# Kernel optimization log

Hardware: AMD Instinct MI355X
Metric: run time of the kernel (lower is better)

## Reference

```python
import jax, jax.numpy as jnp
import numpy as np
import math

B, N, DQ, DK, DV, H = 8, 1024, 512, 512, 512, 8


def setup_inputs() -> dict:
    key = jax.random.key(0)
    ks = jax.random.split(key, 9)
    s = 0.02
    return {
        "Q": jax.random.normal(ks[0], (B, N, DQ), jnp.float32),
        "K": jax.random.normal(ks[1], (B, N, DK), jnp.float32),
        "mask": jax.random.bernoulli(ks[2], 0.9, (B, N)).astype(jnp.float32),
        "Wq": jax.random.normal(ks[3], (DQ, DV), jnp.float32) * s,
        "bq": jnp.zeros((DV,), jnp.float32),
        "Wk": jax.random.normal(ks[4], (DK, DV), jnp.float32) * s,
        "bk": jnp.zeros((DV,), jnp.float32),
        "Wv": jax.random.normal(ks[5], (DK, DV), jnp.float32) * s,
        "bv": jnp.zeros((DV,), jnp.float32),
        "Wo": jax.random.normal(ks[6], (DV, DV), jnp.float32) * s,
        "bo": jnp.zeros((DV,), jnp.float32),
    }


def reference(Q, K, mask, Wq, bq, Wk, bk, Wv, bv, Wo, bo):
    b, n, _ = Q.shape
    dV = Wq.shape[1]
    dh = dV // H
    scale = 1.0 / math.sqrt(dV)
    m = mask[..., None]                      # [B,N,1]
    Qp = (Q @ Wq + bq) * m                   # [B,N,dV]
    Kp = (K @ Wk + bk) * m
    Vp = (K @ Wv + bv) * m
    # torch.cat(x.split(dh,2),0) == head-major stacking -> keep as [H,B,N,dh]
    q = Qp.reshape(b, n, H, dh).transpose(2, 0, 1, 3)
    k = Kp.reshape(b, n, H, dh).transpose(2, 0, 1, 3)
    v = Vp.reshape(b, n, H, dh).transpose(2, 0, 1, 3)
    S = jnp.einsum('hbnd,hbmd->hbnm', q, k) * scale   # [H,B,N,N]
    mx = jnp.max(S, axis=3, keepdims=True)            # unmasked row max (faithful)
    m1 = mask[None, :, :, None]                       # [1,B,N,1]
    m2 = mask[None, :, None, :]                       # [1,B,1,N]
    num = jnp.exp((S - mx) * m1 * m2) * m1 * m2
    A = num / (jnp.sum(num, axis=3, keepdims=True) + 1e-16)
    O = q + jnp.einsum('hbnm,hbmd->hbnd', A, v)       # residual on Q_
    O = O.transpose(1, 2, 0, 3).reshape(b, n, dV)     # un-split heads
    O = O + jax.nn.relu((O @ Wo + bo) * m)
    return O
```

## Files before the change

kernel.cpp:

```cpp
#include <hip/hip_runtime.h>

typedef short bf16x8 __attribute__((ext_vector_type(8)));
typedef float f32x4 __attribute__((ext_vector_type(4)));
typedef float f32x16 __attribute__((ext_vector_type(16)));

#define MFMA16(a, b, c) __builtin_amdgcn_mfma_f32_16x16x32_bf16((a), (b), (c), 0, 0, 0)
#define MFMA32(a, b, c) __builtin_amdgcn_mfma_f32_32x32x16_bf16((a), (b), (c), 0, 0, 0)

#define GLOAD_LDS16(g, l)                                              \
  __builtin_amdgcn_global_load_lds(                                    \
      (const __attribute__((address_space(1))) unsigned int*)(g),      \
      (__attribute__((address_space(3))) unsigned int*)(l), 16, 0, 0)

__device__ __forceinline__ unsigned short f2b(float f) {
  union { float f; unsigned int u; } x; x.f = f;
  unsigned int r = x.u + 0x7FFFu + ((x.u >> 16) & 1u);
  return (unsigned short)(r >> 16);
}
__device__ __forceinline__ float b2f(unsigned short h) {
  union { unsigned int u; float f; } x; x.u = ((unsigned int)h) << 16;
  return x.f;
}
__device__ __forceinline__ unsigned int cvtpk(float lo, float hi) {
  unsigned int r;
  asm("v_cvt_pk_bf16_f32 %0, %1, %2" : "=v"(r) : "v"(lo), "v"(hi));
  return r;
}
__device__ __forceinline__ short cvt1(float x) {
  return (short)(unsigned short)cvtpk(x, x);
}
__device__ __forceinline__ float vexp2(float x) {
  float r;
  asm("v_exp_f32 %0, %1" : "=v"(r) : "v"(x));
  return r;
}

#define SCALE2 0.06375870724f

__global__ __launch_bounds__(256) void prep_kernel(
    const float* __restrict__ Wq, const float* __restrict__ Wk,
    const float* __restrict__ Wv, const float* __restrict__ Wo,
    const float* __restrict__ Q, const float* __restrict__ K,
    const float* __restrict__ mask,
    short* __restrict__ Wt, short* __restrict__ Qb, short* __restrict__ Kb,
    short* __restrict__ mbf) {
  __shared__ float tile[64][65];
  const int bid = blockIdx.x;
  const int t = threadIdx.x;
  if (bid < 256) {
    const int z = bid >> 6;
    const int rem = bid & 63;
    const int k0 = (rem >> 3) * 64, n0 = (rem & 7) * 64;
    const float* W = (z == 0) ? Wq : (z == 1) ? Wk : (z == 2) ? Wv : Wo;
    const float ws = (z == 1) ? SCALE2 : 1.0f;
    const int r = t >> 4, cc = (t & 15) * 4;
#pragma unroll
    for (int it = 0; it < 4; ++it) {
      int row = r + it * 16;
      const float4 v = *(const float4*)(W + (k0 + row) * 512 + n0 + cc);
      tile[row][cc + 0] = v.x; tile[row][cc + 1] = v.y;
      tile[row][cc + 2] = v.z; tile[row][cc + 3] = v.w;
    }
    __syncthreads();
    short* out = Wt + z * (512 * 512);
#pragma unroll
    for (int it = 0; it < 4; ++it) {
      int nrow = r + it * 16;
      unsigned int u0 = cvtpk(tile[cc + 0][nrow] * ws, tile[cc + 1][nrow] * ws);
      unsigned int u1 = cvtpk(tile[cc + 2][nrow] * ws, tile[cc + 3][nrow] * ws);
      uint2 uv; uv.x = u0; uv.y = u1;
      *(uint2*)(out + (n0 + nrow) * 512 + k0 + cc) = uv;
    }
  } else {
    const int idx = bid - 256;
    const int ybit = idx >> 11;
    const int x = idx & 2047;
    if (ybit == 0 && x < 4) {
      int i = (x * 256 + t) * 8;
      float4 a = *(const float4*)(mask + i);
      float4 bb = *(const float4*)(mask + i + 4);
      unsigned int m0 = (a.x != 0.f) ? 0x3F80u : 0u;
      unsigned int m1 = (a.y != 0.f) ? 0x3F80u : 0u;
      unsigned int m2 = (a.z != 0.f) ? 0x3F80u : 0u;
      unsigned int m3 = (a.w != 0.f) ? 0x3F80u : 0u;
      unsigned int m4 = (bb.x != 0.f) ? 0x3F80u : 0u;
      unsigned int m5 = (bb.y != 0.f) ? 0x3F80u : 0u;
      unsigned int m6 = (bb.z != 0.f) ? 0x3F80u : 0u;
      unsigned int m7 = (bb.w != 0.f) ? 0x3F80u : 0u;
      uint4 mm;
      mm.x = m0 | (m1 << 16); mm.y = m2 | (m3 << 16);
      mm.z = m4 | (m5 << 16); mm.w = m6 | (m7 << 16);
      *(uint4*)(mbf + i) = mm;
    }
    const float* src = ybit ? K : Q;
    short* dst = ybit ? Kb : Qb;
    int i = (x * 256 + t) * 8;
    float4 v0 = *(const float4*)(src + i);
    float4 v1 = *(const float4*)(src + i + 4);
    uint2 a, b;
    a.x = cvtpk(v0.x, v0.y); a.y = cvtpk(v0.z, v0.w);
    b.x = cvtpk(v1.x, v1.y); b.y = cvtpk(v1.z, v1.w);
    *(uint2*)(dst + i) = a;
    *(uint2*)(dst + i + 4) = b;
  }
}

__device__ __forceinline__ void gemm_bf16_core(
    const short* __restrict__ A, const short* __restrict__ Wt,
    short* Lb, int m0, int t, f32x4 acc[4][4]) {
  const int lane = t & 63, w = t >> 6;
  const int c = lane & 15, g = lane >> 4;
  const int wr = w >> 1, wc = w & 1;
  const int lr = lane >> 3;
  const int sswz = ((lane & 7) ^ lr) << 3;
  const int swc = (c & 7) << 3;
  short* Al = Lb;
  short* Bl = Lb + 8192;

  for (int kt = 0; kt < 8; ++kt) {
#pragma unroll
    for (int it = 0; it < 4; ++it) {
      int row = w * 32 + it * 8;
      GLOAD_LDS16(A + (size_t)(m0 + row + lr) * 512 + kt * 64 + sswz, Al + row * 64);
      GLOAD_LDS16(Wt + (size_t)(row + lr) * 512 + kt * 64 + sswz, Bl + row * 64);
    }
    __syncthreads();
    __builtin_amdgcn_s_setprio(1);
#pragma unroll
    for (int kc = 0; kc < 2; ++kc) {
      bf16x8 af[4], bfr[4];
#pragma unroll
      for (int mi = 0; mi < 4; ++mi) {
        int r = wr * 64 + mi * 16 + c;
        af[mi] = *(const bf16x8*)(Al + r * 64 + ((kc * 32 + 8 * g) ^ swc));
      }
#pragma unroll
      for (int ni = 0; ni < 4; ++ni) {
        int r = wc * 64 + ni * 16 + c;
        bfr[ni] = *(const bf16x8*)(Bl + r * 64 + ((kc * 32 + 8 * g) ^ swc));
      }
#pragma unroll
      for (int mi = 0; mi < 4; ++mi)
#pragma unroll
        for (int ni = 0; ni < 4; ++ni)
          acc[mi][ni] = MFMA16(af[mi], bfr[ni], acc[mi][ni]);
    }
    __builtin_amdgcn_s_setprio(0);
    __syncthreads();
  }
}

__global__ __launch_bounds__(256) void proj2_kernel(
    const short* __restrict__ Qb, const short* __restrict__ Kb,
    const short* __restrict__ Wt4,
    const float* __restrict__ bq, const float* __restrict__ bk, const float* __restrict__ bv,
    const float* __restrict__ maskf,
    short* __restrict__ Qp, short* __restrict__ Kp, short* __restrict__ Vt) {
  __shared__ short Lbuf[16384];
  const int by = blockIdx.y;
  const int m0 = blockIdx.x * 128;
  const int t = threadIdx.x;
  const short* A;
  const short* Wt;
  const float* bias;
  int nbase;
  if (by < 4) { A = Qb; nbase = by * 128; Wt = Wt4 + nbase * 512; bias = bq; }
  else if (by < 8) { A = Kb; nbase = (by - 4) * 128; Wt = Wt4 + 262144 + nbase * 512; bias = bk; }
  else { A = Kb; nbase = (by - 8) * 128; Wt = Wt4 + 524288 + nbase * 512; bias = bv; }
  const float bscale = (by >= 4 && by < 8) ? SCALE2 : 1.0f;

  const f32x4 zz = {0.f, 0.f, 0.f, 0.f};
  f32x4 acc[4][4];
#pragma unroll
  for (int mi = 0; mi < 4; ++mi)
#pragma unroll
    for (int ni = 0; ni < 4; ++ni) acc[mi][ni] = zz;
  gemm_bf16_core(A, Wt, Lbuf, m0, t, acc);

  const int lane = t & 63, w = t >> 6;
  const int c = lane & 15, g = lane >> 4;
  const int wr = w >> 1, wc = w & 1;
  float mk[4][4];
#pragma unroll
  for (int mi = 0; mi < 4; ++mi) {
    int mbase = m0 + wr * 64 + mi * 16 + 4 * g;
#pragma unroll
    for (int i = 0; i < 4; ++i) mk[mi][i] = maskf[mbase + i];
  }
  float bval[4];
#pragma unroll
  for (int ni = 0; ni < 4; ++ni) bval[ni] = bias[nbase + wc * 64 + ni * 16 + c] * bscale;

  if (by < 8) {
#pragma unroll
    for (int ni = 0; ni < 4; ++ni) {
      int nloc = wc * 64 + ni * 16 + c;
#pragma unroll
      for (int mi = 0; mi < 4; ++mi) {
#pragma unroll
        for (int i = 0; i < 4; ++i) {
          int mloc = wr * 64 + mi * 16 + 4 * g + i;
          float v = (acc[mi][ni][i] + bval[ni]) * mk[mi][i];
          Lbuf[mloc * 128 + (nloc ^ ((mloc & 7) << 3))] = cvt1(v);
        }
      }
    }
    __syncthreads();
    short* outp = (by < 4) ? Qp : Kp;
    const int rrow = t >> 4, rcol = (t & 15) * 8;
#pragma unroll
    for (int p = 0; p < 8; ++p) {
      int m = p * 16 + rrow;
      bf16x8 vv = *(const bf16x8*)(Lbuf + m * 128 + (rcol ^ ((m & 7) << 3)));
      *(bf16x8*)(outp + (size_t)(m0 + m) * 512 + nbase + rcol) = vv;
    }
  } else {
#pragma unroll
    for (int ni = 0; ni < 4; ++ni) {
      int nloc = wc * 64 + ni * 16 + c;
#pragma unroll
      for (int mi = 0; mi < 4; ++mi) {
        int mloc4 = wr * 64 + mi * 16 + 4 * g;
        unsigned int lo = cvtpk((acc[mi][ni][0] + bval[ni]) * mk[mi][0],
                                (acc[mi][ni][1] + bval[ni]) * mk[mi][1]);
        unsigned int hi = cvtpk((acc[mi][ni][2] + bval[ni]) * mk[mi][2],
                                (acc[mi][ni][3] + bval[ni]) * mk[mi][3]);
        int ma = (mloc4 & 15) + (((mloc4 >> 4) ^ (nloc & 7)) << 4);
        uint2 uv; uv.x = lo; uv.y = hi;
        *(uint2*)(Lbuf + nloc * 128 + ma) = uv;
      }
    }
    __syncthreads();
    const int rrow = t >> 4, rcol = (t & 15) * 8;
#pragma unroll
    for (int p = 0; p < 8; ++p) {
      int n = p * 16 + rrow;
      int ma = (rcol & 8) + (((rcol >> 4) ^ (n & 7)) << 4);
      bf16x8 vv = *(const bf16x8*)(Lbuf + n * 128 + ma);
      int d = nbase + n;
      int hh = d >> 6, dd = d & 63;
      int mg = m0 + rcol;
      int bi = mg >> 10, seq0 = mg & 1023;
      *(bf16x8*)(Vt + ((size_t)((bi * 8 + hh) * 64 + dd)) * 1024 + seq0) = vv;
    }
  }
}

__global__ __launch_bounds__(256, 4) void attn8_kernel(
    const short* __restrict__ Qp, const short* __restrict__ Kp,
    const short* __restrict__ Vt, const float* __restrict__ mask,
    const short* __restrict__ mbf, short* __restrict__ Obb) {
  __shared__ short Kl[2][32 * 128];
  __shared__ short Vl[2][32 * 128];
  __shared__ short Ml[1024];
  const int t = threadIdx.x, lane = t & 63, w = t >> 6;
  const int q32 = lane & 31, hi = lane >> 5;
  const int hw = blockIdx.x;
  const int L = (hw & 7) * 64 + (hw >> 3);
  const int qt = L & 7, head = L >> 3;
  const int b = head & 7, h = head >> 3;
  const int n0 = qt * 128 + w * 32;

  const short* Kg = Kp + (size_t)(b * 1024) * 512 + h * 64;
  const short* Vg = Vt + (size_t)((b * 8 + h) * 64) * 1024;

  bf16x8 qf[4];
  {
    const short* qptr = Qp + ((size_t)(b * 1024 + n0 + q32) * 512 + h * 64 + 8 * hi);
#pragma unroll
    for (int kk = 0; kk < 4; ++kk) qf[kk] = *(const bf16x8*)(qptr + 16 * kk);
  }
  asm volatile("s_waitcnt vmcnt(0)" ::: "memory");
  __builtin_amdgcn_sched_barrier(0);

  auto STAGE = [&](int kvt, int buf) {
    const int kr = kvt * 64;
    short* Kd = &Kl[buf][0];
    short* Vd = &Vl[buf][0];
#pragma unroll
    for (int it = 0; it < 2; ++it) {
      int rb = it * 16 + w * 4;
      int r2 = rb + (lane >> 4);
      int sx = (lane & 15) ^ (r2 & 15);
      GLOAD_LDS16(Kg + (size_t)(kr + 2 * r2 + (sx >> 3)) * 512 + (sx & 7) * 8, Kd + rb * 128);
    }
#pragma unroll
    for (int it = 0; it < 2; ++it) {
      int rb = it * 16 + w * 4;
      int rv = rb + (lane >> 4);
      int sx = (lane & 15) ^ (rv & 15);
      GLOAD_LDS16(Vg + (size_t)(2 * rv + (sx >> 3)) * 1024 + kr + (sx & 7) * 8, Vd + rb * 128);
    }
  };

  if (w < 2) GLOAD_LDS16(mbf + b * 1024 + w * 512 + lane * 8, Ml + w * 512);
  STAGE(0, 0);
  STAGE(1, 1);

  f32x16 o0, o1, suma;
#pragma unroll
  for (int e = 0; e < 16; ++e) { o0[e] = 0.f; o1[e] = 0.f; suma[e] = 0.f; }

#pragma unroll 1
  for (int kvt = 0; kvt < 16; ++kvt) {
    const int cur = kvt & 1;
    if (kvt < 15) { asm volatile("s_waitcnt vmcnt(4)" ::: "memory"); }
    else          { asm volatile("s_waitcnt vmcnt(0)" ::: "memory"); }
    __builtin_amdgcn_sched_barrier(0);
    __builtin_amdgcn_s_barrier();
    __builtin_amdgcn_sched_barrier(0);

#pragma unroll
    for (int half = 0; half < 2; ++half) {
      bf16x8 ka[4], va[2][2], mo[2];
      {
        const int kvr = 32 * half + q32;
        const int r2 = kvr >> 1;
#pragma unroll
        for (int kk = 0; kk < 4; ++kk) {
          int sx = ((((kvr & 1) << 3) | (2 * kk + hi)) ^ (r2 & 15));
          ka[kk] = *(const bf16x8*)(&Kl[cur][0] + r2 * 128 + sx * 8);
        }
      }
#pragma unroll
      for (int ds = 0; ds < 2; ++ds) {
        const int d = 32 * ds + q32;
        const int rv = d >> 1;
#pragma unroll
        for (int ch = 0; ch < 2; ++ch) {
          int sx = ((((d & 1) << 3) | (4 * half + 2 * ch + hi)) ^ (rv & 15));
          va[ds][ch] = *(const bf16x8*)(&Vl[cur][0] + rv * 128 + sx * 8);
        }
      }
#pragma unroll
      for (int ch = 0; ch < 2; ++ch)
        mo[ch] = *(const bf16x8*)(Ml + kvt * 64 + 32 * half + 16 * ch + 8 * hi);

      __builtin_amdgcn_sched_barrier(0);
      asm volatile("s_waitcnt lgkmcnt(0)" ::: "memory");
      __builtin_amdgcn_sched_barrier(0);
      if (half == 1) {
        __builtin_amdgcn_s_barrier();
        __builtin_amdgcn_sched_barrier(0);
        if (kvt < 14) STAGE(kvt + 2, cur);
        __builtin_amdgcn_sched_barrier(0);
      }

      f32x16 s0;
#pragma unroll
      for (int e = 0; e < 16; ++e) s0[e] = 0.f;
      __builtin_amdgcn_s_setprio(1);
#pragma unroll
      for (int kk = 0; kk < 4; ++kk) s0 = MFMA32(ka[kk], qf[kk], s0);
      __builtin_amdgcn_s_setprio(0);

      f32x16 p0;
#pragma unroll
      for (int e = 0; e < 16; ++e) p0[e] = vexp2(s0[e]);

      bf16x8 pf[2];
#pragma unroll
      for (int ch = 0; ch < 2; ++ch) {
        unsigned int w01a = cvtpk(p0[8 * ch + 0], p0[8 * ch + 1]);
        unsigned int w01b = cvtpk(p0[8 * ch + 2], p0[8 * ch + 3]);
        unsigned int w23a = cvtpk(p0[8 * ch + 4], p0[8 * ch + 5]);
        unsigned int w23b = cvtpk(p0[8 * ch + 6], p0[8 * ch + 7]);
        unsigned int x0 = hi ? w01a : w23a;
        unsigned int x1 = hi ? w01b : w23b;
        unsigned int g0 = (unsigned int)__shfl_xor((int)x0, 32);
        unsigned int g1 = (unsigned int)__shfl_xor((int)x1, 32);
        union { unsigned int u[4]; bf16x8 v; } pu;
        pu.u[0] = hi ? g0 : w01a;
        pu.u[1] = hi ? g1 : w01b;
        pu.u[2] = hi ? w23a : g0;
        pu.u[3] = hi ? w23b : g1;
        pf[ch] = pu.v;
      }

      __builtin_amdgcn_s_setprio(1);
#pragma unroll
      for (int ch = 0; ch < 2; ++ch) {
        o0 = MFMA32(va[0][ch], pf[ch], o0);
        o1 = MFMA32(va[1][ch], pf[ch], o1);
        suma = MFMA32(mo[ch], pf[ch], suma);
      }
      __builtin_amdgcn_s_setprio(0);
    }
  }

  __builtin_amdgcn_s_barrier();
  __builtin_amdgcn_sched_barrier(0);
  short* Tw = (w < 2) ? (&Kl[0][0] + w * 2304) : (&Vl[0][0] + (w - 2) * 2304);
  const float inv = __builtin_amdgcn_rcpf(suma[0] + 1e-16f);
#pragma unroll
  for (int rr = 0; rr < 4; ++rr) {
    uint2 uv0, uv1;
    uv0.x = cvtpk(o0[4 * rr + 0] * inv, o0[4 * rr + 1] * inv);
    uv0.y = cvtpk(o0[4 * rr + 2] * inv, o0[4 * rr + 3] * inv);
    *(uint2*)(Tw + q32 * 68 + 8 * rr + 4 * hi) = uv0;
    uv1.x = cvtpk(o1[4 * rr + 0] * inv, o1[4 * rr + 1] * inv);
    uv1.y = cvtpk(o1[4 * rr + 2] * inv, o1[4 * rr + 3] * inv);
    *(uint2*)(Tw + q32 * 68 + 32 + 8 * rr + 4 * hi) = uv1;
  }
  asm volatile("s_waitcnt lgkmcnt(0)" ::: "memory");
  __builtin_amdgcn_sched_barrier(0);

  const int erow = lane >> 1, ecs = (lane & 1) * 8;
  const float mk1 = mask[b * 1024 + n0 + erow];
#pragma unroll
  for (int it = 0; it < 4; ++it) {
    int col = ecs + it * 16;
    bf16x8 av = *(const bf16x8*)(Tw + erow * 68 + col);
    const short* qptr = Qp + (size_t)(b * 1024 + n0 + erow) * 512 + h * 64 + col;
    bf16x8 qv = *(const bf16x8*)qptr;
    uint4 rr;
    rr.x = cvtpk(b2f((unsigned short)qv[0]) + mk1 * b2f((unsigned short)av[0]),
                 b2f((unsigned short)qv[1]) + mk1 * b2f((unsigned short)av[1]));
    rr.y = cvtpk(b2f((unsigned short)qv[2]) + mk1 * b2f((unsigned short)av[2]),
                 b2f((unsigned short)qv[3]) + mk1 * b2f((unsigned short)av[3]));
    rr.z = cvtpk(b2f((unsigned short)qv[4]) + mk1 * b2f((unsigned short)av[4]),
                 b2f((unsigned short)qv[5]) + mk1 * b2f((unsigned short)av[5]));
    rr.w = cvtpk(b2f((unsigned short)qv[6]) + mk1 * b2f((unsigned short)av[6]),
                 b2f((unsigned short)qv[7]) + mk1 * b2f((unsigned short)av[7]));
    *(uint4*)(Obb + (size_t)(b * 1024 + n0 + erow) * 512 + h * 64 + col) = rr;
  }
}

__global__ __launch_bounds__(256) void final2_kernel(
    const short* __restrict__ Obb,
    const short* __restrict__ Wto, const float* __restrict__ bo,
    const float* __restrict__ maskf, float* __restrict__ out) {
  __shared__ short Lbuf[16384];
  const int m0 = blockIdx.x * 128, n0 = blockIdx.y * 128;
  const int t = threadIdx.x;
  const f32x4 zz = {0.f, 0.f, 0.f, 0.f};
  f32x4 acc[4][4];
#pragma unroll
  for (int mi = 0; mi < 4; ++mi)
#pragma unroll
    for (int ni = 0; ni < 4; ++ni) acc[mi][ni] = zz;
  gemm_bf16_core(Obb, Wto + n0 * 512, Lbuf, m0, t, acc);

  const int lane = t & 63, w = t >> 6;
  const int c = lane & 15, g = lane >> 4;
  const int wr = w >> 1, wc = w & 1;
  float mk[4][4];
#pragma unroll
  for (int mi = 0; mi < 4; ++mi) {
    int mbase = m0 + wr * 64 + mi * 16 + 4 * g;
#pragma unroll
    for (int i = 0; i < 4; ++i) mk[mi][i] = maskf[mbase + i];
  }
#pragma unroll
  for (int ni = 0; ni < 4; ++ni) {
    int n = n0 + wc * 64 + ni * 16 + c;
    float bval = bo[n];
#pragma unroll
    for (int mi = 0; mi < 4; ++mi) {
      int mbase = m0 + wr * 64 + mi * 16 + 4 * g;
#pragma unroll
      for (int i = 0; i < 4; ++i) {
        float v = (acc[mi][ni][i] + bval) * mk[mi][i];
        v = fmaxf(v, 0.f);
        size_t off = (size_t)(mbase + i) * 512 + n;
        out[off] = b2f((unsigned short)Obb[off]) + v;
      }
    }
  }
}

extern "C" void kernel_launch(void* const* d_in, const int* in_sizes, int n_in,
                              void* d_out, int out_size, void* d_ws, size_t ws_size,
                              hipStream_t stream) {
  (void)in_sizes; (void)n_in; (void)out_size; (void)ws_size;
  const float* Q    = (const float*)d_in[0];
  const float* K    = (const float*)d_in[1];
  const float* mask = (const float*)d_in[2];
  const float* Wq   = (const float*)d_in[3];
  const float* bq   = (const float*)d_in[4];
  const float* Wk   = (const float*)d_in[5];
  const float* bk   = (const float*)d_in[6];
  const float* Wv   = (const float*)d_in[7];
  const float* bv   = (const float*)d_in[8];
  const float* Wo   = (const float*)d_in[9];
  const float* bo   = (const float*)d_in[10];

  char* ws = (char*)d_ws;
  const size_t MB = 1048576;
  short* Wt4 = (short*)ws;
  short* Qb  = (short*)(ws + 2 * MB);
  short* Kb  = (short*)(ws + 10 * MB);
  short* Qp  = (short*)(ws + 18 * MB);
  short* Kp  = (short*)(ws + 26 * MB);
  short* Vt  = (short*)(ws + 34 * MB);
  short* Obb = (short*)(ws + 42 * MB);
  short* mbf = (short*)(ws + 50 * MB);
  float* out = (float*)d_out;

  prep_kernel<<<dim3(4352), 256, 0, stream>>>(Wq, Wk, Wv, Wo, Q, K, mask, Wt4, Qb, Kb, mbf);
  proj2_kernel<<<dim3(64, 12), 256, 0, stream>>>(Qb, Kb, Wt4, bq, bk, bv, mask, Qp, Kp, Vt);
  attn8_kernel<<<dim3(512), 256, 0, stream>>>(Qp, Kp, Vt, mask, mbf, Obb);
  final2_kernel<<<dim3(64, 4), 256, 0, stream>>>(Obb, Wt4 + 3 * 262144, bo, mask, out);
}
```

Measured before the change: 90.96 us.

## Split attention KV range across two waves per 32-query block

The attention kernel now uses 128-thread blocks that each handle 32 queries, with the two waves splitting the 1024-key range in half (split-K). Each wave stages its own K/V tiles into a private LDS buffer. It prefetches only one tile ahead and needs no block barriers in the main loop. Partial O and row-sum accumulators are combined through LDS at the end. This gives 4x more blocks and removes intra-loop barriers, at the cost of re-reading Q-independent K/V per 32 queries (4x more K/V traffic), a shallower prefetch, and an extra reduction step.

```diff
diff --git a/kernel.cpp b/kernel.cpp
--- a/kernel.cpp
+++ b/kernel.cpp
@@ -246,23 +246,25 @@
   }
 }
 
-__global__ __launch_bounds__(256, 4) void attn8_kernel(
+__global__ __launch_bounds__(128, 2) void attn9_kernel(
     const short* __restrict__ Qp, const short* __restrict__ Kp,
     const short* __restrict__ Vt, const float* __restrict__ mask,
     const short* __restrict__ mbf, short* __restrict__ Obb) {
   __shared__ short Kl[2][32 * 128];
   __shared__ short Vl[2][32 * 128];
-  __shared__ short Ml[1024];
+  __shared__ short Ml[2][512];
   const int t = threadIdx.x, lane = t & 63, w = t >> 6;
   const int q32 = lane & 31, hi = lane >> 5;
   const int hw = blockIdx.x;
-  const int L = (hw & 7) * 64 + (hw >> 3);
-  const int qt = L & 7, head = L >> 3;
+  const int L = (hw & 7) * 256 + (hw >> 3);
+  const int qt = L & 31, head = L >> 5;
   const int b = head & 7, h = head >> 3;
-  const int n0 = qt * 128 + w * 32;
-
-  const short* Kg = Kp + (size_t)(b * 1024) * 512 + h * 64;
-  const short* Vg = Vt + (size_t)((b * 8 + h) * 64) * 1024;
+  const int n0 = qt * 32;
+
+  const short* Kg = Kp + (size_t)(b * 1024 + w * 512) * 512 + h * 64;
+  const short* Vg = Vt + (size_t)((b * 8 + h) * 64) * 1024 + w * 512;
+  short* Kw = &Kl[w][0];
+  short* Vw = &Vl[w][0];
 
   bf16x8 qf[4];
   {
@@ -270,95 +272,70 @@
 #pragma unroll
     for (int kk = 0; kk < 4; ++kk) qf[kk] = *(const bf16x8*)(qptr + 16 * kk);
   }
+  GLOAD_LDS16(mbf + b * 1024 + w * 512 + lane * 8, &Ml[w][0]);
   asm volatile("s_waitcnt vmcnt(0)" ::: "memory");
   __builtin_amdgcn_sched_barrier(0);
 
-  auto STAGE = [&](int kvt, int buf) {
+  auto STAGE = [&](int kvt) {
     const int kr = kvt * 64;
-    short* Kd = &Kl[buf][0];
-    short* Vd = &Vl[buf][0];
-#pragma unroll
-    for (int it = 0; it < 2; ++it) {
-      int rb = it * 16 + w * 4;
+#pragma unroll
+    for (int it = 0; it < 8; ++it) {
+      int rb = it * 4;
       int r2 = rb + (lane >> 4);
       int sx = (lane & 15) ^ (r2 & 15);
-      GLOAD_LDS16(Kg + (size_t)(kr + 2 * r2 + (sx >> 3)) * 512 + (sx & 7) * 8, Kd + rb * 128);
-    }
-#pragma unroll
-    for (int it = 0; it < 2; ++it) {
-      int rb = it * 16 + w * 4;
+      GLOAD_LDS16(Kg + (size_t)(kr + 2 * r2 + (sx >> 3)) * 512 + (sx & 7) * 8, Kw + rb * 128);
+    }
+#pragma unroll
+    for (int it = 0; it < 8; ++it) {
+      int rb = it * 4;
       int rv = rb + (lane >> 4);
       int sx = (lane & 15) ^ (rv & 15);
-      GLOAD_LDS16(Vg + (size_t)(2 * rv + (sx >> 3)) * 1024 + kr + (sx & 7) * 8, Vd + rb * 128);
+      GLOAD_LDS16(Vg + (size_t)(2 * rv + (sx >> 3)) * 1024 + kr + (sx & 7) * 8, Vw + rb * 128);
     }
   };
 
-  if (w < 2) GLOAD_LDS16(mbf + b * 1024 + w * 512 + lane * 8, Ml + w * 512);
-  STAGE(0, 0);
-  STAGE(1, 1);
+  STAGE(0);
 
   f32x16 o0, o1, suma;
 #pragma unroll
   for (int e = 0; e < 16; ++e) { o0[e] = 0.f; o1[e] = 0.f; suma[e] = 0.f; }
 
 #pragma unroll 1
-  for (int kvt = 0; kvt < 16; ++kvt) {
-    const int cur = kvt & 1;
-    if (kvt < 15) { asm volatile("s_waitcnt vmcnt(4)" ::: "memory"); }
-    else          { asm volatile("s_waitcnt vmcnt(0)" ::: "memory"); }
-    __builtin_amdgcn_sched_barrier(0);
-    __builtin_amdgcn_s_barrier();
-    __builtin_amdgcn_sched_barrier(0);
-
+  for (int kvt = 0; kvt < 8; ++kvt) {
+    asm volatile("s_waitcnt vmcnt(8)" ::: "memory");
+    __builtin_amdgcn_sched_barrier(0);
+
+    bf16x8 ka[2][4], mo[2][2];
 #pragma unroll
     for (int half = 0; half < 2; ++half) {
-      bf16x8 ka[4], va[2][2], mo[2];
-      {
-        const int kvr = 32 * half + q32;
-        const int r2 = kvr >> 1;
-#pragma unroll
-        for (int kk = 0; kk < 4; ++kk) {
-          int sx = ((((kvr & 1) << 3) | (2 * kk + hi)) ^ (r2 & 15));
-          ka[kk] = *(const bf16x8*)(&Kl[cur][0] + r2 * 128 + sx * 8);
-        }
-      }
-#pragma unroll
-      for (int ds = 0; ds < 2; ++ds) {
-        const int d = 32 * ds + q32;
-        const int rv = d >> 1;
-#pragma unroll
-        for (int ch = 0; ch < 2; ++ch) {
-          int sx = ((((d & 1) << 3) | (4 * half + 2 * ch + hi)) ^ (rv & 15));
-          va[ds][ch] = *(const bf16x8*)(&Vl[cur][0] + rv * 128 + sx * 8);
-        }
+      const int kvr = 32 * half + q32;
+      const int r2 = kvr >> 1;
+#pragma unroll
+      for (int kk = 0; kk < 4; ++kk) {
+        int sx = ((((kvr & 1) << 3) | (2 * kk + hi)) ^ (r2 & 15));
+        ka[half][kk] = *(const bf16x8*)(Kw + r2 * 128 + sx * 8);
       }
 #pragma unroll
       for (int ch = 0; ch < 2; ++ch)
-        mo[ch] = *(const bf16x8*)(Ml + kvt * 64 + 32 * half + 16 * ch + 8 * hi);
-
-      __builtin_amdgcn_sched_barrier(0);
-      asm volatile("s_waitcnt lgkmcnt(0)" ::: "memory");
-      __builtin_amdgcn_sched_barrier(0);
-      if (half == 1) {
-        __builtin_amdgcn_s_barrier();
-        __builtin_amdgcn_sched_barrier(0);
-        if (kvt < 14) STAGE(kvt + 2, cur);
-        __builtin_amdgcn_sched_barrier(0);
-      }
-
+        mo[half][ch] = *(const bf16x8*)(&Ml[w][0] + kvt * 64 + 32 * half + 16 * ch + 8 * hi);
+    }
+    __builtin_amdgcn_sched_barrier(0);
+    asm volatile("s_waitcnt lgkmcnt(0)" ::: "memory");
+    __builtin_amdgcn_sched_barrier(0);
+
+    bf16x8 pf[2][2];
+#pragma unroll
+    for (int half = 0; half < 2; ++half) {
       f32x16 s0;
 #pragma unroll
       for (int e = 0; e < 16; ++e) s0[e] = 0.f;
       __builtin_amdgcn_s_setprio(1);
 #pragma unroll
-      for (int kk = 0; kk < 4; ++kk) s0 = MFMA32(ka[kk], qf[kk], s0);
+      for (int kk = 0; kk < 4; ++kk) s0 = MFMA32(ka[half][kk], qf[kk], s0);
       __builtin_amdgcn_s_setprio(0);
-
       f32x16 p0;
 #pragma unroll
       for (int e = 0; e < 16; ++e) p0[e] = vexp2(s0[e]);
-
-      bf16x8 pf[2];
 #pragma unroll
       for (int ch = 0; ch < 2; ++ch) {
         unsigned int w01a = cvtpk(p0[8 * ch + 0], p0[8 * ch + 1]);
@@ -374,55 +351,97 @@
         pu.u[1] = hi ? g1 : w01b;
         pu.u[2] = hi ? w23a : g0;
         pu.u[3] = hi ? w23b : g1;
-        pf[ch] = pu.v;
-      }
-
-      __builtin_amdgcn_s_setprio(1);
+        pf[half][ch] = pu.v;
+      }
+    }
+
+    asm volatile("s_waitcnt vmcnt(0)" ::: "memory");
+    __builtin_amdgcn_sched_barrier(0);
+    bf16x8 va[2][2][2];
+#pragma unroll
+    for (int ds = 0; ds < 2; ++ds) {
+      const int d = 32 * ds + q32;
+      const int rv = d >> 1;
+#pragma unroll
+      for (int half = 0; half < 2; ++half)
+#pragma unroll
+        for (int ch = 0; ch < 2; ++ch) {
+          int sx = ((((d & 1) << 3) | (4 * half + 2 * ch + hi)) ^ (rv & 15));
+          va[half][ds][ch] = *(const bf16x8*)(Vw + rv * 128 + sx * 8);
+        }
+    }
+    __builtin_amdgcn_sched_barrier(0);
+    asm volatile("s_waitcnt lgkmcnt(0)" ::: "memory");
+    __builtin_amdgcn_sched_barrier(0);
+
+    if (kvt < 7) STAGE(kvt + 1);
+    __builtin_amdgcn_sched_barrier(0);
+
+    __builtin_amdgcn_s_setprio(1);
+#pragma unroll
+    for (int half = 0; half < 2; ++half)
 #pragma unroll
       for (int ch = 0; ch < 2; ++ch) {
-        o0 = MFMA32(va[0][ch], pf[ch], o0);
-        o1 = MFMA32(va[1][ch], pf[ch], o1);
-        suma = MFMA32(mo[ch], pf[ch], suma);
-      }
-      __builtin_amdgcn_s_setprio(0);
-    }
-  }
-
-  __builtin_amdgcn_s_barrier();
-  __builtin_amdgcn_sched_barrier(0);
-  short* Tw = (w < 2) ? (&Kl[0][0] + w * 2304) : (&Vl[0][0] + (w - 2) * 2304);
-  const float inv = __builtin_amdgcn_rcpf(suma[0] + 1e-16f);
-#pragma unroll
-  for (int rr = 0; rr < 4; ++rr) {
-    uint2 uv0, uv1;
-    uv0.x = cvtpk(o0[4 * rr + 0] * inv, o0[4 * rr + 1] * inv);
-    uv0.y = cvtpk(o0[4 * rr + 2] * inv, o0[4 * rr + 3] * inv);
-    *(uint2*)(Tw + q32 * 68 + 8 * rr + 4 * hi) = uv0;
-    uv1.x = cvtpk(o1[4 * rr + 0] * inv, o1[4 * rr + 1] * inv);
-    uv1.y = cvtpk(o1[4 * rr + 2] * inv, o1[4 * rr + 3] * inv);
-    *(uint2*)(Tw + q32 * 68 + 32 + 8 * rr + 4 * hi) = uv1;
-  }
-  asm volatile("s_waitcnt lgkmcnt(0)" ::: "memory");
-  __builtin_amdgcn_sched_barrier(0);
-
-  const int erow = lane >> 1, ecs = (lane & 1) * 8;
-  const float mk1 = mask[b * 1024 + n0 + erow];
-#pragma unroll
-  for (int it = 0; it < 4; ++it) {
-    int col = ecs + it * 16;
-    bf16x8 av = *(const bf16x8*)(Tw + erow * 68 + col);
-    const short* qptr = Qp + (size_t)(b * 1024 + n0 + erow) * 512 + h * 64 + col;
-    bf16x8 qv = *(const bf16x8*)qptr;
-    uint4 rr;
-    rr.x = cvtpk(b2f((unsigned short)qv[0]) + mk1 * b2f((unsigned short)av[0]),
-                 b2f((unsigned short)qv[1]) + mk1 * b2f((unsigned short)av[1]));
-    rr.y = cvtpk(b2f((unsigned short)qv[2]) + mk1 * b2f((unsigned short)av[2]),
-                 b2f((unsigned short)qv[3]) + mk1 * b2f((unsigned short)av[3]));
-    rr.z = cvtpk(b2f((unsigned short)qv[4]) + mk1 * b2f((unsigned short)av[4]),
-                 b2f((unsigned short)qv[5]) + mk1 * b2f((unsigned short)av[5]));
-    rr.w = cvtpk(b2f((unsigned short)qv[6]) + mk1 * b2f((unsigned short)av[6]),
-                 b2f((unsigned short)qv[7]) + mk1 * b2f((unsigned short)av[7]));
-    *(uint4*)(Obb + (size_t)(b * 1024 + n0 + erow) * 512 + h * 64 + col) = rr;
+        o0 = MFMA32(va[half][0][ch], pf[half][ch], o0);
+        o1 = MFMA32(va[half][1][ch], pf[half][ch], o1);
+        suma = MFMA32(mo[half][ch], pf[half][ch], suma);
+      }
+    __builtin_amdgcn_s_setprio(0);
+  }
+
+  if (w == 1) {
+    float* po = (float*)&Kl[1][0];
+    float* ps = (float*)&Vl[1][0];
+#pragma unroll
+    for (int e = 0; e < 16; ++e) {
+      po[e * 64 + lane] = o0[e];
+      po[(16 + e) * 64 + lane] = o1[e];
+    }
+    ps[lane] = suma[0];
+  }
+  __syncthreads();
+  if (w == 0) {
+    const float* po = (const float*)&Kl[1][0];
+    const float* ps = (const float*)&Vl[1][0];
+#pragma unroll
+    for (int e = 0; e < 16; ++e) {
+      o0[e] += po[e * 64 + lane];
+      o1[e] += po[(16 + e) * 64 + lane];
+    }
+    const float inv = __builtin_amdgcn_rcpf(suma[0] + ps[lane] + 1e-16f);
+    short* Tw = &Vl[0][0];
+#pragma unroll
+    for (int rr = 0; rr < 4; ++rr) {
+      uint2 uv0, uv1;
+      uv0.x = cvtpk(o0[4 * rr + 0] * inv, o0[4 * rr + 1] * inv);
+      uv0.y = cvtpk(o0[4 * rr + 2] * inv, o0[4 * rr + 3] * inv);
+      *(uint2*)(Tw + q32 * 68 + 8 * rr + 4 * hi) = uv0;
+      uv1.x = cvtpk(o1[4 * rr + 0] * inv, o1[4 * rr + 1] * inv);
+      uv1.y = cvtpk(o1[4 * rr + 2] * inv, o1[4 * rr + 3] * inv);
+      *(uint2*)(Tw + q32 * 68 + 32 + 8 * rr + 4 * hi) = uv1;
+    }
+    asm volatile("s_waitcnt lgkmcnt(0)" ::: "memory");
+    __builtin_amdgcn_sched_barrier(0);
+
+    const int erow = lane >> 1, ecs = (lane & 1) * 8;
+    const float mk1 = mask[b * 1024 + n0 + erow];
+#pragma unroll
+    for (int it = 0; it < 4; ++it) {
+      int col = ecs + it * 16;
+      bf16x8 av = *(const bf16x8*)(Tw + erow * 68 + col);
+      const short* qptr = Qp + (size_t)(b * 1024 + n0 + erow) * 512 + h * 64 + col;
+      bf16x8 qv = *(const bf16x8*)qptr;
+      uint4 rr;
+      rr.x = cvtpk(b2f((unsigned short)qv[0]) + mk1 * b2f((unsigned short)av[0]),
+                   b2f((unsigned short)qv[1]) + mk1 * b2f((unsigned short)av[1]));
+      rr.y = cvtpk(b2f((unsigned short)qv[2]) + mk1 * b2f((unsigned short)av[2]),
+                   b2f((unsigned short)qv[3]) + mk1 * b2f((unsigned short)av[3]));
+      rr.z = cvtpk(b2f((unsigned short)qv[4]) + mk1 * b2f((unsigned short)av[4]),
+                   b2f((unsigned short)qv[5]) + mk1 * b2f((unsigned short)av[5]));
+      rr.w = cvtpk(b2f((unsigned short)qv[6]) + mk1 * b2f((unsigned short)av[6]),
+                   b2f((unsigned short)qv[7]) + mk1 * b2f((unsigned short)av[7]));
+      *(uint4*)(Obb + (size_t)(b * 1024 + n0 + erow) * 512 + h * 64 + col) = rr;
+    }
   }
 }
 
@@ -499,6 +518,6 @@
 
   prep_kernel<<<dim3(4352), 256, 0, stream>>>(Wq, Wk, Wv, Wo, Q, K, mask, Wt4, Qb, Kb, mbf);
   proj2_kernel<<<dim3(64, 12), 256, 0, stream>>>(Qb, Kb, Wt4, bq, bk, bv, mask, Qp, Kp, Vt);
-  attn8_kernel<<<dim3(512), 256, 0, stream>>>(Qp, Kp, Vt, mask, mbf, Obb);
+  attn9_kernel<<<dim3(2048), 128, 0, stream>>>(Qp, Kp, Vt, mask, mbf, Obb);
   final2_kernel<<<dim3(64, 4), 256, 0, stream>>>(Obb, Wt4 + 3 * 262144, bo, mask, out);
 }
```

New measurement: 85.95 us. 5.5% less time.
